# Kernel tuning notes

Measured on AMD Instinct MI355X. Metric: run time of the kernel, lower is better.

The kernel has to match this reference:

```python
import jax, jax.numpy as jnp
import numpy as np
from jax import lax

M, G = 16, 4
INP = 256
OUP = 256
K = 3
EPS = 1e-5


def _weightnet(x, gap_vec, fc1_w, fc1_b, fc2_w, inp, oup, stride):
    # x: [B, inp, H, W], gap_vec: [B, 16]
    B, _, H, W = x.shape
    a = jax.nn.sigmoid(gap_vec @ fc1_w.T + fc1_b)          # [B, M*oup]
    groups = G * oup                                        # 1024
    out_pg = (oup * inp * K * K) // groups                  # 576
    in_pg = (M * oup) // groups                             # 4
    a = a.reshape(B, groups, in_pg)
    w2 = fc2_w.reshape(groups, out_pg, in_pg)
    # grouped 1x1 conv generating per-sample conv weights
    xw = jnp.einsum('bgi,goi->bgo', a, w2)                  # [B, groups, out_pg]
    xw = xw.reshape(B * oup, inp, K, K)                     # per-sample kernels
    xr = x.reshape(1, B * inp, H, W)
    out = lax.conv_general_dilated(
        xr, xw, (stride, stride), [(1, 1), (1, 1)],
        dimension_numbers=('NCHW', 'OIHW', 'NCHW'),
        feature_group_count=B)
    return out.reshape(B, oup, out.shape[2], out.shape[3])


def _bn(x, g, b, m, v):
    scale = (g / jnp.sqrt(v + EPS))[:, None, None]
    return (x - m[:, None, None]) * scale + b[:, None, None]


def setup_inputs() -> dict:
    key = jax.random.key(0)
    ks = jax.random.split(key, 20)
    d = {}
    d['x'] = jax.random.normal(ks[0], (32, 256, 56, 56), jnp.float32)
    d['reduce_w'] = jax.random.normal(ks[1], (16, 256), jnp.float32) * 0.05
    d['reduce_b'] = jax.random.normal(ks[2], (16,), jnp.float32) * 0.05
    d['w1_fc1_w'] = jax.random.normal(ks[3], (4096, 16), jnp.float32) * 0.05
    d['w1_fc1_b'] = jax.random.normal(ks[4], (4096,), jnp.float32) * 0.05
    d['w1_fc2_w'] = jax.random.normal(ks[5], (589824, 4), jnp.float32) * 0.05
    d['bn1_g'] = jax.random.uniform(ks[6], (256,), jnp.float32) + 0.5
    d['bn1_b'] = jax.random.normal(ks[7], (256,), jnp.float32) * 0.05
    d['bn1_m'] = jax.random.normal(ks[8], (256,), jnp.float32) * 0.05
    d['bn1_v'] = jax.random.uniform(ks[9], (256,), jnp.float32) + 0.5
    d['w2_fc1_w'] = jax.random.normal(ks[10], (4096, 16), jnp.float32) * 0.05
    d['w2_fc1_b'] = jax.random.normal(ks[11], (4096,), jnp.float32) * 0.05
    d['w2_fc2_w'] = jax.random.normal(ks[12], (589824, 4), jnp.float32) * 0.05
    d['bn2_g'] = jax.random.uniform(ks[13], (256,), jnp.float32) + 0.5
    d['bn2_b'] = jax.random.normal(ks[14], (256,), jnp.float32) * 0.05
    d['bn2_m'] = jax.random.normal(ks[15], (256,), jnp.float32) * 0.05
    d['bn2_v'] = jax.random.uniform(ks[16], (256,), jnp.float32) + 0.5
    return d


def reference(x, reduce_w, reduce_b, w1_fc1_w, w1_fc1_b, w1_fc2_w,
              bn1_g, bn1_b, bn1_m, bn1_v,
              w2_fc1_w, w2_fc1_b, w2_fc2_w,
              bn2_g, bn2_b, bn2_m, bn2_v):
    # global average pool -> reduce 1x1 conv
    gap = x.mean(axis=(2, 3))                       # [B, in_planes]
    gap = gap @ reduce_w.T + reduce_b               # [B, 16]
    out = _weightnet(x, gap, w1_fc1_w, w1_fc1_b, w1_fc2_w, INP, OUP, 1)
    out = jax.nn.relu(_bn(out, bn1_g, bn1_b, bn1_m, bn1_v))
    out = _weightnet(out, gap, w2_fc1_w, w2_fc1_b, w2_fc2_w, OUP, OUP, 1)
    out = _bn(out, bn2_g, bn2_b, bn2_m, bn2_v)
    out = out + x                                   # identity shortcut (stride=1, in==out)
    return jax.nn.relu(out)
```

## Files before the change

kernel.cpp:

```cpp
#include <hip/hip_runtime.h>

typedef short bf16x8 __attribute__((ext_vector_type(8)));
typedef float f32x4 __attribute__((ext_vector_type(4)));

#define EPSV 1e-5f
#define BNUM 32
#define CH 256
#define HW 3136
#define PXT 3684
#define NCHUNK 32
#define PERB_SHORTS (NCHUNK*PXT*8)
#define WB_PERB 589824

__device__ __forceinline__ unsigned short f2bf(float f) {
  unsigned int u = __float_as_uint(f);
  u += 0x7fffu + ((u >> 16) & 1u);
  return (unsigned short)(u >> 16);
}

__device__ __forceinline__ void gld16(const void* g, void* l) {
  __builtin_amdgcn_global_load_lds((const __attribute__((address_space(1))) void*)g,
                                   (__attribute__((address_space(3))) void*)l,
                                   16, 0, 0);
}

__global__ void k_gapc(const float* __restrict__ x, float* __restrict__ gapc) {
  int bc = blockIdx.x;
  const float4* p4 = (const float4*)(x + (size_t)bc * HW);
  int t = threadIdx.x;
  float s = 0.f;
  for (int i = t; i < 784; i += 256) {
    float4 v = p4[i];
    s += v.x + v.y + v.z + v.w;
  }
  for (int off = 32; off; off >>= 1) s += __shfl_down(s, off, 64);
  __shared__ float red[4];
  int lane = t & 63, wv = t >> 6;
  if (lane == 0) red[wv] = s;
  __syncthreads();
  if (t == 0) gapc[bc] = (red[0] + red[1] + red[2] + red[3]) * (1.f / 3136.f);
}

__global__ void k_gap16(const float* __restrict__ gapc, const float* __restrict__ rw,
                        const float* __restrict__ rb, float* __restrict__ g16) {
  int t = threadIdx.x;
  int b = t >> 4, j = t & 15;
  const float* gc = gapc + b * 256;
  const float* w = rw + j * 256;
  float s = rb[j];
  for (int c = 0; c < 256; ++c) s += gc[c] * w[c];
  g16[t] = s;
}

__global__ void k_act(const float* __restrict__ g16,
                      const float* __restrict__ w1w, const float* __restrict__ w1b,
                      const float* __restrict__ w2w, const float* __restrict__ w2b,
                      float* __restrict__ a1, float* __restrict__ a2) {
  int idx = blockIdx.x * 256 + threadIdx.x;
  int which = idx >> 17;
  int r = idx & 131071;
  int b = r >> 12, m = r & 4095;
  const float* w = (which ? w2w : w1w) + m * 16;
  float s = which ? w2b[m] : w1b[m];
  const float* g = g16 + b * 16;
#pragma unroll
  for (int j = 0; j < 16; ++j) s += g[j] * w[j];
  float out = 1.f / (1.f + __expf(-s));
  (which ? a2 : a1)[r] = out;
}

__global__ void k_zero(unsigned short* __restrict__ xp1, unsigned short* __restrict__ xp2) {
  int bc = blockIdx.x;
  int t = threadIdx.x;
  uint4 z = {0u, 0u, 0u, 0u};
  for (int wbuf = 0; wbuf < 2; ++wbuf) {
    unsigned short* base = (wbuf ? xp2 : xp1) + (size_t)bc * (PXT * 8);
    uint4* p = (uint4*)base;
    if (t < 123) p[t] = z;
    p[3370 + t] = z;
    if (t < 58) p[3626 + t] = z;
    if (t < 56) {
      int e = 64 + (t + 1) * 58 + 57;
      p[e] = z;
      p[e + 1] = z;
    }
  }
}

__global__ void k_xpad(const float* __restrict__ x, unsigned short* __restrict__ xp) {
  int y = blockIdx.x, ch = blockIdx.y, b = blockIdx.z;
  int l = threadIdx.x;
  if (l >= 56) return;
  const float* src = x + ((size_t)(b * 256 + ch * 8)) * HW + y * 56 + l;
  ushort4 lo, hi;
  lo.x = f2bf(src[0 * HW]); lo.y = f2bf(src[1 * HW]);
  lo.z = f2bf(src[2 * HW]); lo.w = f2bf(src[3 * HW]);
  hi.x = f2bf(src[4 * HW]); hi.y = f2bf(src[5 * HW]);
  hi.z = f2bf(src[6 * HW]); hi.w = f2bf(src[7 * HW]);
  unsigned short* dst = xp + ((size_t)(b * NCHUNK + ch)) * (PXT * 8)
                           + (size_t)(64 + (y + 1) * 58 + (l + 1)) * 8;
  *(ushort4*)dst = lo;
  *(ushort4*)(dst + 4) = hi;
}

__global__ void k_wgen(const float* __restrict__ a, const float4* __restrict__ w2,
                       unsigned short* __restrict__ wb) {
  int og = blockIdx.x & 63, bg = blockIdx.x >> 6;
  int t = threadIdx.x;
  for (int bi = 0; bi < 4; ++bi) {
    int b = bg * 4 + bi;
    const float* ab = a + b * 4096;
    unsigned short* wbb = wb + (size_t)b * WB_PERB;
    for (int it = 0; it < 36; ++it) {
      int wi = it * 256 + t;
      int oc_l = wi / 2304;
      int r = wi - oc_l * 2304;
      int ic = r / 9;
      int k9 = r - ic * 9;
      int kh = k9 / 3;
      int kw = k9 - kh * 3;
      int oc = og * 4 + oc_l;
      int g = oc * 4 + (ic >> 6);
      int o = (ic & 63) * 9 + k9;
      float4 w4 = w2[g * 576 + o];
      float4 a4 = *(const float4*)(ab + g * 4);
      float s = w4.x * a4.x + w4.y * a4.y + w4.z * a4.z + w4.w * a4.w;
      wbb[kh * 196608 + (ic >> 3) * 6144 + oc * 24 + kw * 8 + (ic & 7)] = f2bf(s);
    }
  }
}

__global__ __launch_bounds__(512, 1)
void k_conv(const unsigned short* __restrict__ xpad,
            const unsigned short* __restrict__ wbuf,
            const float* __restrict__ bgp, const float* __restrict__ bbp,
            const float* __restrict__ bmp, const float* __restrict__ bvp,
            const float* __restrict__ resid,
            unsigned short* __restrict__ outpad,
            float* __restrict__ outf,
            const int mode) {
  __shared__ unsigned short sW[2][24576];
  __shared__ unsigned short sX[2][8192];

  const int tid = threadIdx.x;
  const int lane = tid & 63;
  const int wv = tid >> 6;
  const int wocg = wv >> 1;
  const int wpxg = wv & 1;
  const int ocl = lane & 15;
  const int kc = lane >> 4;

  int rid = blockIdx.x;
  int xcd = rid & 7;
  int j = rid >> 3;
  int b = xcd + 8 * (j / 15);
  int slot = j % 15;
  int p0 = 58 + slot * 224;

  const unsigned short* xb = xpad + (size_t)b * PERB_SHORTS + 64 * 8;
  const unsigned short* wbb = wbuf + (size_t)b * WB_PERB;

  f32x4 acc[4][7];
#pragma unroll
  for (int i = 0; i < 4; ++i)
#pragma unroll
    for (int k = 0; k < 7; ++k)
      acc[i][k] = (f32x4){0.f, 0.f, 0.f, 0.f};

  auto STAGE = [&](int t, int buf) {
    int s = t >> 2;
    s = t / 3;
    int kh = t - s * 3;
    const unsigned short* wsrc = wbb + (size_t)(kh * 8 + s) * 24576;
#pragma unroll
    for (int i = 0; i < 6; ++i) {
      int seg = wv * 6 + i;
      gld16(wsrc + seg * 512 + lane * 8, &sW[buf][seg * 512]);
    }
    int q0 = p0 + kh * 58 - 59;
    int chunk = wv >> 1, half = wv & 1;
    const unsigned short* xs = xb + ((long)(s * 4 + chunk) * PXT + q0 + half * 128) * 8;
#pragma unroll
    for (int i = 0; i < 2; ++i)
      gld16(xs + (i * 64 + lane) * 8, &sX[buf][chunk * 2048 + half * 1024 + i * 512]);
  };

  STAGE(0, 0);
  int cur = 0;
  for (int t = 0; t < 24; ++t) {
    if (t + 1 < 24) {
      STAGE(t + 1, cur ^ 1);
      asm volatile("s_waitcnt vmcnt(8)" ::: "memory");
    } else {
      asm volatile("s_waitcnt vmcnt(0)" ::: "memory");
    }
    __builtin_amdgcn_s_barrier();
    __builtin_amdgcn_sched_barrier(0);
#pragma unroll
    for (int kw = 0; kw < 3; ++kw) {
      bf16x8 af[4], bfr[7];
#pragma unroll
      for (int fm = 0; fm < 4; ++fm)
        af[fm] = *(const bf16x8*)&sW[cur][kc * 6144 + (wocg * 64 + fm * 16 + ocl) * 24 + kw * 8];
#pragma unroll
      for (int fn = 0; fn < 7; ++fn)
        bfr[fn] = *(const bf16x8*)&sX[cur][kc * 2048 + (wpxg * 112 + fn * 16 + ocl + kw) * 8];
      __builtin_amdgcn_s_setprio(1);
#pragma unroll
      for (int fm = 0; fm < 4; ++fm)
#pragma unroll
        for (int fn = 0; fn < 7; ++fn)
          acc[fm][fn] = __builtin_amdgcn_mfma_f32_16x16x32_bf16(af[fm], bfr[fn], acc[fm][fn], 0, 0, 0);
      __builtin_amdgcn_s_setprio(0);
    }
    __builtin_amdgcn_s_barrier();
    cur ^= 1;
  }

  __syncthreads();
  float* scb = (float*)&sX[0][0];
  if (tid < 256) {
    float sc = bgp[tid] * rsqrtf(bvp[tid] + EPSV);
    scb[tid] = sc;
    scb[256 + tid] = bbp[tid] - bmp[tid] * sc;
  }
  __syncthreads();

  const int dpb = wpxg * 112 + ocl;
  if (mode == 1) {
#pragma unroll
    for (int fn = 0; fn < 7; ++fn) {
      int pp = p0 + dpb + fn * 16;
      int py = pp / 58;
      int px = pp - py * 58;
      if (py < 1 || py > 56 || px < 1 || px > 56) continue;
#pragma unroll
      for (int fm = 0; fm < 4; ++fm) {
        int loc = wocg * 64 + fm * 16 + kc * 4;
        f32x4 v = acc[fm][fn];
        ushort4 w;
        w.x = f2bf(fmaxf(v[0] * scb[loc + 0] + scb[256 + loc + 0], 0.f));
        w.y = f2bf(fmaxf(v[1] * scb[loc + 1] + scb[256 + loc + 1], 0.f));
        w.z = f2bf(fmaxf(v[2] * scb[loc + 2] + scb[256 + loc + 2], 0.f));
        w.w = f2bf(fmaxf(v[3] * scb[loc + 3] + scb[256 + loc + 3], 0.f));
        *(ushort4*)&outpad[((size_t)(b * NCHUNK + (loc >> 3))) * (PXT * 8)
                           + (size_t)(64 + pp) * 8 + (loc & 7)] = w;
      }
    }
  } else {
#pragma unroll
    for (int fn = 0; fn < 7; ++fn) {
      int pp = p0 + dpb + fn * 16;
      int py = pp / 58;
      int px = pp - py * 58;
      if (py < 1 || py > 56 || px < 1 || px > 56) continue;
      int obase = (py - 1) * 56 + (px - 1);
#pragma unroll
      for (int fm = 0; fm < 4; ++fm) {
        int loc = wocg * 64 + fm * 16 + kc * 4;
        f32x4 v = acc[fm][fn];
#pragma unroll
        for (int r = 0; r < 4; ++r) {
          int oc = loc + r;
          size_t oi = ((size_t)(b * CH + oc)) * HW + obase;
          float tv = v[r] * scb[oc] + scb[256 + oc] + resid[oi];
          outf[oi] = fmaxf(tv, 0.f);
        }
      }
    }
  }
}

#define OFF_XP1 ((size_t)0)
#define XP_BYTES ((size_t)BNUM * PERB_SHORTS * 2)
#define OFF_XP2 (OFF_XP1 + XP_BYTES)
#define OFF_WB  (OFF_XP2 + XP_BYTES)
#define WB_BYTES ((size_t)BNUM * WB_PERB * 2)
#define OFF_GAPC (OFF_WB + WB_BYTES)
#define OFF_G16  (OFF_GAPC + 32768)
#define OFF_A1   (OFF_G16 + 2048)
#define OFF_A2   (OFF_A1 + 524288)

extern "C" void kernel_launch(void* const* d_in, const int* in_sizes, int n_in,
                              void* d_out, int out_size, void* d_ws, size_t ws_size,
                              hipStream_t stream) {
  (void)in_sizes; (void)n_in; (void)out_size; (void)ws_size;
  const float* x        = (const float*)d_in[0];
  const float* reduce_w = (const float*)d_in[1];
  const float* reduce_b = (const float*)d_in[2];
  const float* w1fc1w   = (const float*)d_in[3];
  const float* w1fc1b   = (const float*)d_in[4];
  const float* w1fc2w   = (const float*)d_in[5];
  const float* bn1g     = (const float*)d_in[6];
  const float* bn1b     = (const float*)d_in[7];
  const float* bn1m     = (const float*)d_in[8];
  const float* bn1v     = (const float*)d_in[9];
  const float* w2fc1w   = (const float*)d_in[10];
  const float* w2fc1b   = (const float*)d_in[11];
  const float* w2fc2w   = (const float*)d_in[12];
  const float* bn2g     = (const float*)d_in[13];
  const float* bn2b     = (const float*)d_in[14];
  const float* bn2m     = (const float*)d_in[15];
  const float* bn2v     = (const float*)d_in[16];

  char* ws = (char*)d_ws;
  unsigned short* xp1 = (unsigned short*)(ws + OFF_XP1);
  unsigned short* xp2 = (unsigned short*)(ws + OFF_XP2);
  unsigned short* wb  = (unsigned short*)(ws + OFF_WB);
  float* gapc = (float*)(ws + OFF_GAPC);
  float* g16  = (float*)(ws + OFF_G16);
  float* a1   = (float*)(ws + OFF_A1);
  float* a2   = (float*)(ws + OFF_A2);
  float* outf = (float*)d_out;

  k_gapc<<<BNUM * CH, 256, 0, stream>>>(x, gapc);
  k_gap16<<<1, 512, 0, stream>>>(gapc, reduce_w, reduce_b, g16);
  k_act<<<1024, 256, 0, stream>>>(g16, w1fc1w, w1fc1b, w2fc1w, w2fc1b, a1, a2);
  k_zero<<<1024, 256, 0, stream>>>(xp1, xp2);
  k_xpad<<<dim3(56, NCHUNK, BNUM), 64, 0, stream>>>(x, xp1);

  k_wgen<<<512, 256, 0, stream>>>(a1, (const float4*)w1fc2w, wb);
  k_conv<<<480, 512, 0, stream>>>(xp1, wb, bn1g, bn1b, bn1m, bn1v,
                                  nullptr, xp2, nullptr, 1);
  k_wgen<<<512, 256, 0, stream>>>(a2, (const float4*)w2fc2w, wb);
  k_conv<<<480, 512, 0, stream>>>(xp2, wb, bn2g, bn2b, bn2m, bn2v,
                                  x, nullptr, outf, 2);
}
```

Before: 466.3 us.

## Interleave next-stage LDS prefetch into the MFMA loop and parallelize gap16 reduction

The conv main loop no longer issues the whole next stage's global-to-LDS loads up front. It splits the weight and activation loads across the kw sub-iterations, waits on all outstanding loads at the top of each step, and adds a barrier plus an lgkmcnt wait before each MFMA burst. The aim is to spread memory issue among the compute and reduce stalls. The cost is a full vmcnt(0) wait each step and an extra barrier per kw, which could serialize loads with compute. Separately, the tiny gap16 kernel now uses one block per sample with a 32-lane shuffle reduction instead of a single block doing serial 256-length dot products.

```diff
diff --git a/kernel.cpp b/kernel.cpp
--- a/kernel.cpp
+++ b/kernel.cpp
@@ -43,13 +43,17 @@
 
 __global__ void k_gap16(const float* __restrict__ gapc, const float* __restrict__ rw,
                         const float* __restrict__ rb, float* __restrict__ g16) {
+  int b = blockIdx.x;
   int t = threadIdx.x;
-  int b = t >> 4, j = t & 15;
+  int j = t >> 5;
+  int c0 = t & 31;
   const float* gc = gapc + b * 256;
   const float* w = rw + j * 256;
-  float s = rb[j];
-  for (int c = 0; c < 256; ++c) s += gc[c] * w[c];
-  g16[t] = s;
+  float s = 0.f;
+#pragma unroll
+  for (int k = 0; k < 8; ++k) s += gc[c0 + k * 32] * w[c0 + k * 32];
+  for (int off = 16; off; off >>= 1) s += __shfl_down(s, off, 32);
+  if (c0 == 0) g16[b * 16 + j] = s + rb[j];
 }
 
 __global__ void k_act(const float* __restrict__ g16,
@@ -167,16 +171,18 @@
     for (int k = 0; k < 7; ++k)
       acc[i][k] = (f32x4){0.f, 0.f, 0.f, 0.f};
 
-  auto STAGE = [&](int t, int buf) {
-    int s = t >> 2;
-    s = t / 3;
+  auto STAGE_W = [&](int t, int buf, int i0, int i1) {
+    int s = t / 3;
     int kh = t - s * 3;
     const unsigned short* wsrc = wbb + (size_t)(kh * 8 + s) * 24576;
-#pragma unroll
-    for (int i = 0; i < 6; ++i) {
+    for (int i = i0; i < i1; ++i) {
       int seg = wv * 6 + i;
       gld16(wsrc + seg * 512 + lane * 8, &sW[buf][seg * 512]);
     }
+  };
+  auto STAGE_X = [&](int t, int buf) {
+    int s = t / 3;
+    int kh = t - s * 3;
     int q0 = p0 + kh * 58 - 59;
     int chunk = wv >> 1, half = wv & 1;
     const unsigned short* xs = xb + ((long)(s * 4 + chunk) * PXT + q0 + half * 128) * 8;
@@ -185,17 +191,13 @@
       gld16(xs + (i * 64 + lane) * 8, &sX[buf][chunk * 2048 + half * 1024 + i * 512]);
   };
 
-  STAGE(0, 0);
+  STAGE_W(0, 0, 0, 6);
+  STAGE_X(0, 0);
   int cur = 0;
   for (int t = 0; t < 24; ++t) {
-    if (t + 1 < 24) {
-      STAGE(t + 1, cur ^ 1);
-      asm volatile("s_waitcnt vmcnt(8)" ::: "memory");
-    } else {
-      asm volatile("s_waitcnt vmcnt(0)" ::: "memory");
-    }
+    asm volatile("s_waitcnt vmcnt(0)" ::: "memory");
     __builtin_amdgcn_s_barrier();
-    __builtin_amdgcn_sched_barrier(0);
+    const bool pre = (t + 1) < 24;
 #pragma unroll
     for (int kw = 0; kw < 3; ++kw) {
       bf16x8 af[4], bfr[7];
@@ -205,6 +207,10 @@
 #pragma unroll
       for (int fn = 0; fn < 7; ++fn)
         bfr[fn] = *(const bf16x8*)&sX[cur][kc * 2048 + (wpxg * 112 + fn * 16 + ocl + kw) * 8];
+      if (kw == 0 && pre) STAGE_W(t + 1, cur ^ 1, 0, 4);
+      if (kw == 1 && pre) { STAGE_W(t + 1, cur ^ 1, 4, 6); STAGE_X(t + 1, cur ^ 1); }
+      __builtin_amdgcn_s_barrier();
+      asm volatile("s_waitcnt lgkmcnt(0)" ::: "memory");
       __builtin_amdgcn_s_setprio(1);
 #pragma unroll
       for (int fm = 0; fm < 4; ++fm)
@@ -213,7 +219,6 @@
           acc[fm][fn] = __builtin_amdgcn_mfma_f32_16x16x32_bf16(af[fm], bfr[fn], acc[fm][fn], 0, 0, 0);
       __builtin_amdgcn_s_setprio(0);
     }
-    __builtin_amdgcn_s_barrier();
     cur ^= 1;
   }
 
@@ -314,7 +319,7 @@
   float* outf = (float*)d_out;
 
   k_gapc<<<BNUM * CH, 256, 0, stream>>>(x, gapc);
-  k_gap16<<<1, 512, 0, stream>>>(gapc, reduce_w, reduce_b, g16);
+  k_gap16<<<BNUM, 512, 0, stream>>>(gapc, reduce_w, reduce_b, g16);
   k_act<<<1024, 256, 0, stream>>>(g16, w1fc1w, w1fc1b, w2fc1w, w2fc1b, a1, a2);
   k_zero<<<1024, 256, 0, stream>>>(xp1, xp2);
   k_xpad<<<dim3(56, NCHUNK, BNUM), 64, 0, stream>>>(x, xp1);
```

New measurement: 421.2 us. 9.7% less time.
